# Kernel tuning notes

Measured on AMD Instinct MI355X. Metric: run time of the kernel, lower is better.

Reference implementation:

```python
import jax, jax.numpy as jnp
import numpy as np

B, T, V, D, C, d, TSZ, L, P = 8, 12, 512, 1, 128, 8, 3, 3, 12
BETA = TSZ - 1


def _gauss(emb, mu, isg):
    # Gaussian_component: sum over d of -0.5*(emb-mu)^2 * inv_sigma^2
    return jnp.sum(-0.5 * (emb - mu) ** 2 * isg ** 2, axis=-1)


def _gfs(h, fw, fb, gw, gb):
    # GFS: Conv2d(T->C, kernel (1,C)) over x[B,T,V,C] -> [B,C,V], then 1x1 GLU
    s = jnp.einsum('btvc,otc->bov', h, fw) + fb[None, :, None]
    g = jnp.einsum('bov,po->bpv', s, gw) + gb[None, :, None]
    lhs, rhs = jnp.split(g, 2, axis=1)
    return lhs * jax.nn.sigmoid(rhs)  # B,C,V


def _forward(x, sape, tape, srpe, trpe, zeros_x, zeros_tape, range_mask,
             input_w, input_b, fs0_fc_w, fs0_fc_b, fs0_glu_w, fs0_glu_b,
             mus, inv_sigmas, xproj_w, xproj_b, seproj_w, teproj_w, ln_g, ln_b,
             fs_fc_w, fs_fc_b, fs_glu_w, fs_glu_b, glu_w, glu_b, out_w, out_b):
    h = x @ input_w + input_b  # B,T,V,C (InputLayer)
    tape_pad = jnp.concatenate([zeros_tape, tape], axis=1)  # B,T+beta,1,d
    mask = range_mask.reshape(V, TSZ, V)  # [j, k, i]
    skips = [_gfs(h, fs0_fc_w, fs0_fc_b, fs0_glu_w, fs0_glu_b)]
    for l in range(L):
        h_pad = jnp.concatenate([zeros_x, h], axis=1)  # B,T+beta,V,C
        # all T shifted windows at once (vectorizes the per-timestep loop)
        xwin = jnp.stack([h_pad[:, k:k + T] for k in range(TSZ)], axis=2)     # B,T,k,V,C
        twin = jnp.stack([tape_pad[:, k:k + T] for k in range(TSZ)], axis=2)  # B,T,k,1,d
        mu, isg = mus[l], inv_sigmas[l]
        gi = _gauss(sape, mu[0], isg[0])              # (V,)   source node i
        gj = _gauss(sape, mu[1], isg[1])              # (V,)   target node j
        gti = _gauss(tape, mu[2], isg[2])[:, :, 0]    # (B,T)  tape_i
        gtj = _gauss(twin, mu[3], isg[3])[..., 0]     # (B,T,k) tape_j windows
        ge = _gauss(srpe, mu[4], isg[4])              # (V,V)  [i,j]
        gtr = _gauss(trpe, mu[5], isg[5])[:, 0]       # (k,)
        # log S[b,t,j,k,i]; original gaussian[b,k,i,j] -> reshape -> transpose gives S[b,j,(k,i)]
        logS = (gi[None, None, None, None, :] + gj[None, None, :, None, None]
                + gti[:, :, None, None, None] + gtj[:, :, None, :, None]
                + ge.T[None, None, :, None, :] + gtr[None, None, None, :, None])
        S = jnp.exp(logS) * mask[None, None]          # B,T,V(j),k,V(i)
        # STPGConv: bmm(S, x) over the (k,i) axis
        agg = jnp.einsum('btjki,btkic->btjc', S, xwin)  # B,T,V,C
        z = agg @ xproj_w[l] + xproj_b[l]               # B,T,V,2C
        z = z + sape @ seproj_w[l] + tape @ teproj_w[l]  # SE:(V,2C); TE:(B,T,1,2C) broadcasts over V
        mn = jnp.mean(z, axis=-1, keepdims=True)
        var = jnp.mean((z - mn) ** 2, axis=-1, keepdims=True)
        z = (z - mn) * jax.lax.rsqrt(var + 1e-5) * ln_g[l] + ln_b[l]
        lhs, rhs = jnp.split(z, 2, axis=-1)
        h = lhs * jax.nn.sigmoid(rhs)                   # B,T,V,C
        skips.append(_gfs(h, fs_fc_w[l], fs_fc_b[l], fs_glu_w[l], fs_glu_b[l]))
    hc = jnp.concatenate(skips, axis=1)                 # B,(L+1)*C,V
    g = jnp.einsum('bov,po->bpv', hc, glu_w) + glu_b[None, :, None]
    lhs, rhs = jnp.split(g, 2, axis=1)
    gated = lhs * jax.nn.sigmoid(rhs)                   # B,4C,V
    out = jnp.einsum('bov,po->bpv', gated, out_w) + out_b[None, :, None]  # B,P*D,V
    return out[:, :, :, None]                           # D==1 -> (B,P,V,1)


def setup_inputs() -> dict:
    key = jax.random.key(0)

    def nrm(i, shape, s=1.0):
        return s * jax.random.normal(jax.random.fold_in(key, i), shape, dtype=jnp.float32)

    inp = {
        'x': nrm(0, (B, T, V, D)),
        'sape': nrm(1, (V, d), 0.5),
        'tape': nrm(2, (B, T, 1, d), 0.5),
        'srpe': nrm(3, (V, V, d), 0.5),
        'trpe': nrm(4, (TSZ, 1, d), 0.5),
        'zeros_x': jnp.zeros((B, BETA, V, C), jnp.float32),
        'zeros_tape': jnp.zeros((B, BETA, 1, d), jnp.float32),
        'range_mask': (jax.random.uniform(jax.random.fold_in(key, 5), (V, TSZ * V)) < 0.7).astype(jnp.float32),
        'input_w': nrm(6, (D, C), 0.5),
        'input_b': jnp.zeros((C,), jnp.float32),
        'fs0_fc_w': nrm(7, (C, T, C), 1.0 / np.sqrt(T * C)),
        'fs0_fc_b': jnp.zeros((C,), jnp.float32),
        'fs0_glu_w': nrm(8, (2 * C, C), 1.0 / np.sqrt(C)),
        'fs0_glu_b': jnp.zeros((2 * C,), jnp.float32),
        'mus': nrm(9, (L, 6, d)),
        'inv_sigmas': nrm(10, (L, 6, d), 0.3),
        'xproj_w': nrm(11, (L, C, 2 * C), 1.0 / np.sqrt(C)),
        'xproj_b': jnp.zeros((L, 2 * C), jnp.float32),
        'seproj_w': nrm(12, (L, d, 2 * C), 1.0 / np.sqrt(d)),
        'teproj_w': nrm(13, (L, d, 2 * C), 1.0 / np.sqrt(d)),
        'ln_g': jnp.ones((L, 2 * C), jnp.float32),
        'ln_b': jnp.zeros((L, 2 * C), jnp.float32),
        'fs_fc_w': nrm(14, (L, C, T, C), 1.0 / np.sqrt(T * C)),
        'fs_fc_b': jnp.zeros((L, C), jnp.float32),
        'fs_glu_w': nrm(15, (L, 2 * C, C), 1.0 / np.sqrt(C)),
        'fs_glu_b': jnp.zeros((L, 2 * C), jnp.float32),
        'glu_w': nrm(16, (8 * C, 4 * C), 1.0 / np.sqrt(4 * C)),
        'glu_b': jnp.zeros((8 * C,), jnp.float32),
        'out_w': nrm(17, (P * D, 4 * C), 1.0 / np.sqrt(4 * C)),
        'out_b': jnp.zeros((P * D,), jnp.float32),
    }
    return inp


def reference(x, sape, tape, srpe, trpe, zeros_x, zeros_tape, range_mask,
              input_w, input_b, fs0_fc_w, fs0_fc_b, fs0_glu_w, fs0_glu_b,
              mus, inv_sigmas, xproj_w, xproj_b, seproj_w, teproj_w, ln_g, ln_b,
              fs_fc_w, fs_fc_b, fs_glu_w, fs_glu_b, glu_w, glu_b, out_w, out_b):
    return _forward(x, sape, tape, srpe, trpe, zeros_x, zeros_tape, range_mask,
                    input_w, input_b, fs0_fc_w, fs0_fc_b, fs0_glu_w, fs0_glu_b,
                    mus, inv_sigmas, xproj_w, xproj_b, seproj_w, teproj_w, ln_g, ln_b,
                    fs_fc_w, fs_fc_b, fs_glu_w, fs_glu_b, glu_w, glu_b, out_w, out_b)
```

## Files before the change

kernel.cpp:

```cpp
#include <hip/hip_runtime.h>
#include <cstddef>


#define BB 8
#define TT 12
#define VV 512
#define CC 128

typedef unsigned short ushort_t;
typedef float f32x4 __attribute__((ext_vector_type(4)));
typedef short bf16x8 __attribute__((ext_vector_type(8)));

__device__ __forceinline__ float sigmoidf_(float x){ return 1.0f/(1.0f+expf(-x)); }

__device__ __forceinline__ void split_bf16(float x, ushort_t& hi, ushort_t& lo){
  unsigned u = __float_as_uint(x);
  hi = (ushort_t)(u >> 16);
  float r = x - __uint_as_float(u & 0xFFFF0000u);
  lo = (ushort_t)(__float_as_uint(r) >> 16);
}

__device__ __forceinline__ float gauss8(const float* __restrict__ e,
                                        const float* __restrict__ mu,
                                        const float* __restrict__ sg){
  float a = 0.f;
  #pragma unroll
  for (int dd=0; dd<8; ++dd){
    float df = e[dd]-mu[dd];
    float s  = sg[dd];
    a = fmaf(-0.5f*df*df, s*s, a);
  }
  return a;
}

__global__ __launch_bounds__(256) void k_prep(
    const float* __restrict__ fs0_fc_w, const float* __restrict__ fs_fc_w,
    const float* __restrict__ fs0_glu_w, const float* __restrict__ fs_glu_w,
    const float* __restrict__ glu_w, const float* __restrict__ out_w,
    const float* __restrict__ xw, const float* __restrict__ sw,
    const float* __restrict__ tw, const float* __restrict__ xb2,
    float* __restrict__ fwT, float* __restrict__ gwT,
    float* __restrict__ gluT, float* __restrict__ outT,
    ushort_t* __restrict__ xcat_hi, ushort_t* __restrict__ xcat_lo){
  int job = blockIdx.y;
  int gid = blockIdx.x*256 + threadIdx.x;
  if (job < 4){
    if (gid >= 196608) return;
    const float* src = (job==0) ? fs0_fc_w : fs_fc_w + (size_t)(job-1)*196608;
    float* dst = fwT + (size_t)job*196608;
    int r = gid / 1536, c = gid % 1536;
    dst[(size_t)c*128 + r] = src[gid];
  } else if (job < 8){
    if (gid >= 32768) return;
    int sl = job-4;
    const float* src = (sl==0) ? fs0_glu_w : fs_glu_w + (size_t)(sl-1)*32768;
    float* dst = gwT + (size_t)sl*32768;
    int r = gid / 128, c = gid % 128;
    dst[(size_t)c*256 + r] = src[gid];
  } else if (job == 8){
    if (gid >= 524288) return;
    int r = gid / 512, c = gid % 512;
    gluT[(size_t)c*1024 + r] = glu_w[gid];
  } else if (job == 9){
    if (gid >= 6144) return;
    int r = gid / 512, c = gid % 512;
    outT[(size_t)c*12 + r] = out_w[gid];
  } else {
    if (gid >= 122880) return;
    int ll  = gid / 40960;
    int rem = gid - ll*40960;
    int col = rem / 160;
    int k   = rem - col*160;
    float val;
    if (k < 128)       val = xw[(size_t)ll*32768 + (size_t)k*256 + col];
    else if (k < 136)  val = sw[(size_t)ll*2048 + (size_t)(k-128)*256 + col];
    else if (k < 144)  val = tw[(size_t)ll*2048 + (size_t)(k-136)*256 + col];
    else if (k == 144) val = xb2[ll*256 + col];
    else               val = 0.f;
    ushort_t hi, lo; split_bf16(val, hi, lo);
    xcat_hi[gid] = hi;
    xcat_lo[gid] = lo;
  }
}

__global__ __launch_bounds__(256) void k_input(const float* __restrict__ x,
    const float* __restrict__ iw, const float* __restrict__ ib,
    float* __restrict__ hA, ushort_t* __restrict__ hhiT, ushort_t* __restrict__ hloT){
  int bt = blockIdx.x;
  int v0 = blockIdx.y*64;
  int c = threadIdx.x >> 1, half = threadIdx.x & 1;
  int vb = v0 + half*32;
  float wc = iw[c], bc = ib[c];
  const float* xp = x + (size_t)bt*VV + vb;
  float hv[32];
  #pragma unroll
  for (int u=0;u<32;++u) hv[u] = fmaf(xp[u], wc, bc);
  #pragma unroll
  for (int u=0;u<32;++u) hA[((size_t)bt*VV + vb + u)*CC + c] = hv[u];
  unsigned wh[16], wl[16];
  #pragma unroll
  for (int m=0;m<16;++m){
    ushort_t h0,l0,h1,l1;
    split_bf16(hv[2*m],   h0, l0);
    split_bf16(hv[2*m+1], h1, l1);
    wh[m] = (unsigned)h0 | ((unsigned)h1<<16);
    wl[m] = (unsigned)l0 | ((unsigned)l1<<16);
  }
  ushort_t* hp = hhiT + ((size_t)bt*CC + c)*VV + vb;
  ushort_t* lp = hloT + ((size_t)bt*CC + c)*VV + vb;
  #pragma unroll
  for (int q=0;q<4;++q){
    *(uint4*)(hp + q*8) = make_uint4(wh[q*4],wh[q*4+1],wh[q*4+2],wh[q*4+3]);
    *(uint4*)(lp + q*8) = make_uint4(wl[q*4],wl[q*4+1],wl[q*4+2],wl[q*4+3]);
  }
}

__global__ __launch_bounds__(256) void k_gfs1(const float* __restrict__ h,
    const float* __restrict__ fwT, float* __restrict__ s_part){
  int vt = blockIdx.x, b = blockIdx.y, ts = blockIdx.z;
  int tid = threadIdx.x;
  int v0 = vt*32;
  __shared__ float hT[32][34];
  int vtt = tid & 3, ot = tid >> 2;
  float acc[2][8];
  #pragma unroll
  for (int a=0;a<2;++a)
    #pragma unroll
    for (int u=0;u<8;++u) acc[a][u] = 0.f;

  for (int tt=0; tt<3; ++tt){
    int t = ts*3 + tt;
    const float* hbase = h + ((size_t)(b*TT+t)*VV)*CC;
    for (int cch=0; cch<4; ++cch){
      int c0 = cch*32;
      __syncthreads();
      { int vv = tid>>3, c4 = tid&7;
        float4 val = *(const float4*)(hbase + (size_t)(v0+vv)*CC + c0 + c4*4);
        hT[c4*4+0][vv]=val.x; hT[c4*4+1][vv]=val.y;
        hT[c4*4+2][vv]=val.z; hT[c4*4+3][vv]=val.w; }
      __syncthreads();
      const float* fwb = fwT + ((size_t)t*128 + c0)*128 + ot*2;
      for (int c=0;c<32;++c){
        float2 wv = *(const float2*)(fwb + (size_t)c*128);
        float hv[8];
        *(float4*)hv     = *(const float4*)&hT[c][vtt*8];
        *(float4*)(hv+4) = *(const float4*)&hT[c][vtt*8+4];
        #pragma unroll
        for (int u=0;u<8;++u){
          acc[0][u] = fmaf(wv.x, hv[u], acc[0][u]);
          acc[1][u] = fmaf(wv.y, hv[u], acc[1][u]);
        }
      }
    }
  }
  float* sp = s_part + (((size_t)ts*BB+b)*128 + ot*2)*VV + v0 + vtt*8;
  #pragma unroll
  for (int a=0;a<2;++a){
    *(float4*)(sp + (size_t)a*VV)     = *(float4*)&acc[a][0];
    *(float4*)(sp + (size_t)a*VV + 4) = *(float4*)&acc[a][4];
  }
}

__global__ __launch_bounds__(256) void k_gfs2(const float* __restrict__ s_part,
    const float* __restrict__ fb, const float* __restrict__ gwT,
    const float* __restrict__ gb, float* __restrict__ hc, int slot){
  int vt = blockIdx.x, b = blockIdx.y;
  int v0 = vt*32; int tid = threadIdx.x;
  __shared__ float sL[128][36];
  for (int u=0;u<16;++u){
    int lid = u*256 + tid; int o = lid>>5, vv = lid&31;
    float sum = fb[o];
    #pragma unroll
    for (int sp=0;sp<4;++sp)
      sum += s_part[(((size_t)sp*BB+b)*128 + o)*VV + v0 + vv];
    sL[o][vv] = sum;
  }
  __syncthreads();
  int oo = tid & 127, vg = tid >> 7;
  float accL[16], accR[16];
  #pragma unroll
  for (int u=0;u<16;++u){ accL[u]=0.f; accR[u]=0.f; }
  for (int op=0; op<128; ++op){
    float glv = gwT[(size_t)op*256 + oo];
    float grv = gwT[(size_t)op*256 + 128 + oo];
    float sv[16];
    #pragma unroll
    for (int q=0;q<4;++q) *(float4*)(sv+q*4) = *(const float4*)&sL[op][vg*16 + q*4];
    #pragma unroll
    for (int u=0;u<16;++u){ accL[u]=fmaf(glv,sv[u],accL[u]); accR[u]=fmaf(grv,sv[u],accR[u]); }
  }
  float bl = gb[oo], br = gb[128+oo];
  float outv[16];
  #pragma unroll
  for (int u=0;u<16;++u) outv[u] = (accL[u]+bl)*sigmoidf_(accR[u]+br);
  float* dst = hc + ((size_t)b*512 + slot*128 + oo)*VV + v0 + vg*16;
  #pragma unroll
  for (int q=0;q<4;++q) *(float4*)(dst+q*4) = *(float4*)(outv+q*4);
}

__global__ void k_smalls(const float* __restrict__ sape, const float* __restrict__ tape,
    const float* __restrict__ trpe, const float* __restrict__ mus,
    const float* __restrict__ isgs, int l,
    float* __restrict__ gi, float* __restrict__ gj,
    float* __restrict__ E, float* __restrict__ F, float* __restrict__ gtr){
  int tid = threadIdx.x;
  const float* mu = mus  + (size_t)l*48;
  const float* sg = isgs + (size_t)l*48;
  if (tid < 512){
    const float* e = sape + (size_t)tid*8;
    gi[tid] = gauss8(e, mu+0,  sg+0);
    gj[tid] = gauss8(e, mu+8,  sg+8);
  }
  if (tid < 96)
    E[tid] = expf(gauss8(tape + (size_t)tid*8, mu+16, sg+16));
  if (tid < 288){
    int k = tid % 3, bt = tid / 3;
    int t = bt % TT, b = bt / TT;
    int s = t + k - 2;
    F[tid] = (s >= 0) ? expf(gauss8(tape + (size_t)(b*TT+s)*8, mu+24, sg+24)) : 0.f;
  }
  if (tid < 3)
    gtr[tid] = gauss8(trpe + (size_t)tid*8, mu+40, sg+40);
}

__global__ __launch_bounds__(256) void k_W(const float* __restrict__ srpe,
    const float* __restrict__ mask, const float* __restrict__ mus,
    const float* __restrict__ isgs, int l,
    const float* __restrict__ gi, const float* __restrict__ gj,
    const float* __restrict__ gtr,
    ushort_t* __restrict__ Whi, ushort_t* __restrict__ Wlo){
  int it = blockIdx.x, jt = blockIdx.y;
  int tid = threadIdx.x;
  int ii = tid & 15, jj = tid >> 4;
  int i = it*16 + ii, j = jt*16 + jj;
  const float* mu = mus  + (size_t)l*48 + 32;
  const float* sg = isgs + (size_t)l*48 + 32;
  float ge = gauss8(srpe + ((size_t)i*VV + j)*8, mu, sg);
  float base = gi[i] + gj[j] + ge;
  float gk[3] = {gtr[0], gtr[1], gtr[2]};
  __shared__ unsigned tile[16][17];
  int arr = tid>>7, rem = tid&127, jr = rem>>3, p = rem&7;
  for (int k=0;k<3;++k){
    float m = mask[(size_t)j*1536 + k*512 + i];
    float val = m * expf(base + gk[k]);
    ushort_t hi, lo; split_bf16(val, hi, lo);
    __syncthreads();
    tile[jj][ii] = (unsigned)hi | ((unsigned)lo<<16);
    __syncthreads();
    unsigned w0 = tile[jr][2*p], w1 = tile[jr][2*p+1];
    unsigned outw = (arr==0) ? ((w0&0xFFFFu) | (w1<<16))
                             : ((w0>>16) | (w1&0xFFFF0000u));
    ushort_t* dst = (arr ? Wlo : Whi) + ((size_t)k*VV + jt*16 + jr)*VV + it*16 + 2*p;
    *(unsigned*)dst = outw;
  }
}

__global__ __launch_bounds__(256) void k_stpg(
    const ushort_t* __restrict__ hhiT, const ushort_t* __restrict__ hloT,
    const ushort_t* __restrict__ Whi,  const ushort_t* __restrict__ Wlo,
    const float* __restrict__ E, const float* __restrict__ F,
    float* __restrict__ agg){
  int bt = blockIdx.x; int b = bt/TT, t = bt - b*TT;
  int j0 = blockIdx.y * 128;
  int tid = threadIdx.x;
  int lane = tid & 63, wid = tid >> 6;
  int jw = (wid>>1)*64, cw = (wid&1)*64;

  __shared__ ushort_t Ahi_s[128*40];
  __shared__ ushort_t Alo_s[128*40];
  __shared__ ushort_t Bhi_s[128*40];
  __shared__ ushort_t Blo_s[128*40];

  f32x4 acc[4][4];
  #pragma unroll
  for (int a=0;a<4;++a)
    #pragma unroll
    for (int u=0;u<4;++u) acc[a][u] = (f32x4){0.f,0.f,0.f,0.f};

  int kmin = (t>=2) ? 0 : (2-t);
  float Fk[3] = {F[bt*3+0], F[bt*3+1], F[bt*3+2]};
  float Eb = E[bt];

  int ro = (lane&15)*40 + (lane>>4)*8;

  for (int k=kmin; k<3; ++k){
    int s = t + k - 2;
    const ushort_t* gAhi = Whi  + ((size_t)k*VV + j0)*VV;
    const ushort_t* gAlo = Wlo  + ((size_t)k*VV + j0)*VV;
    const ushort_t* gBhi = hhiT + (size_t)(b*TT+s)*CC*VV;
    const ushort_t* gBlo = hloT + (size_t)(b*TT+s)*CC*VV;
    for (int i0=0; i0<512; i0+=32){
      __syncthreads();
      #pragma unroll
      for (int p=0;p<2;++p){
        int sl = p*256 + tid;
        int r = sl>>2, q = sl&3;
        size_t go = (size_t)r*VV + i0 + q*8;
        int lo_ = r*40 + q*8;
        *(uint4*)&Ahi_s[lo_] = *(const uint4*)(gAhi + go);
        *(uint4*)&Alo_s[lo_] = *(const uint4*)(gAlo + go);
        *(uint4*)&Bhi_s[lo_] = *(const uint4*)(gBhi + go);
        *(uint4*)&Blo_s[lo_] = *(const uint4*)(gBlo + go);
      }
      __syncthreads();
      bf16x8 ah[4], al[4], bh[4], bl[4];
      #pragma unroll
      for (int f=0; f<4; ++f){
        ah[f] = *(const bf16x8*)&Ahi_s[(jw + f*16)*40 + ro];
        al[f] = *(const bf16x8*)&Alo_s[(jw + f*16)*40 + ro];
        bh[f] = *(const bf16x8*)&Bhi_s[(cw + f*16)*40 + ro];
        bl[f] = *(const bf16x8*)&Blo_s[(cw + f*16)*40 + ro];
      }
      #pragma unroll
      for (int jf=0;jf<4;++jf)
        #pragma unroll
        for (int cf=0;cf<4;++cf){
          acc[jf][cf] = __builtin_amdgcn_mfma_f32_16x16x32_bf16(ah[jf], bh[cf], acc[jf][cf],0,0,0);
          acc[jf][cf] = __builtin_amdgcn_mfma_f32_16x16x32_bf16(ah[jf], bl[cf], acc[jf][cf],0,0,0);
          acc[jf][cf] = __builtin_amdgcn_mfma_f32_16x16x32_bf16(al[jf], bh[cf], acc[jf][cf],0,0,0);
        }
    }
    if (k < 2){
      float r = Fk[k]/Fk[k+1];
      #pragma unroll
      for (int jf=0;jf<4;++jf)
        #pragma unroll
        for (int cf=0;cf<4;++cf) acc[jf][cf] *= r;
    }
  }
  float fin = Fk[2]*Eb;
  #pragma unroll
  for (int jf=0;jf<4;++jf){
    #pragma unroll
    for (int cf=0;cf<4;++cf){
      int row = j0 + jw + jf*16 + (lane>>4)*4;
      int col = cw + cf*16 + (lane&15);
      float* dst = agg + ((size_t)bt*VV + row)*CC + col;
      #pragma unroll
      for (int e=0;e<4;++e) dst[(size_t)e*CC] = acc[jf][cf][e]*fin;
    }
  }
}

__global__ __launch_bounds__(256,2) void k_xln2(
    float* __restrict__ hA,
    const ushort_t* __restrict__ xcat_hi, const ushort_t* __restrict__ xcat_lo,
    const float* __restrict__ sape, const float* __restrict__ tape,
    const float* __restrict__ lng, const float* __restrict__ lnb, int l,
    ushort_t* __restrict__ hhiT, ushort_t* __restrict__ hloT){
  int vt = blockIdx.x, bt = blockIdx.y;
  int v0 = vt*128;
  int tid = threadIdx.x;
  int lane = tid & 63, w = tid >> 6;
  int l15 = lane & 15, l4 = lane >> 4;
  int ko = l4*8;

  __shared__ float sef[128][8];
  __shared__ float tef[8];
  __shared__ float lnwS[256], lnbS[256];
  { int r2 = tid>>1, hh = tid&1;
    *(float4*)&sef[r2][hh*4] = *(const float4*)(sape + (size_t)(v0+r2)*8 + hh*4); }
  if (tid < 8) tef[tid] = tape[(size_t)bt*8 + tid];
  lnwS[tid] = lng[l*256 + tid];
  lnbS[tid] = lnb[l*256 + tid];
  __syncthreads();

  f32x4 acc[2][16];
  #pragma unroll
  for (int m=0;m<2;++m)
    #pragma unroll
    for (int n=0;n<16;++n) acc[m][n] = (f32x4){0.f,0.f,0.f,0.f};

  const ushort_t* bhb = xcat_hi + (size_t)l*40960;
  const ushort_t* blb = xcat_lo + (size_t)l*40960;

  #pragma unroll
  for (int ks=0; ks<5; ++ks){
    bf16x8 a_h[2], a_l[2];
    #pragma unroll
    for (int m=0;m<2;++m){
      int lrow = w*32 + m*16 + l15;
      float av[8];
      if (ks < 4){
        const float* ap = hA + ((size_t)bt*VV + v0 + lrow)*CC + ks*32 + ko;
        *(float4*)av     = *(const float4*)ap;
        *(float4*)(av+4) = *(const float4*)(ap+4);
      } else {
        #pragma unroll
        for (int u=0;u<8;++u) av[u] = 0.f;
        if (l4==0){
          #pragma unroll
          for (int u=0;u<8;++u) av[u] = sef[lrow][u];
        } else if (l4==1){
          #pragma unroll
          for (int u=0;u<8;++u) av[u] = tef[u];
        } else if (l4==2){
          av[0] = 1.f;
        }
      }
      #pragma unroll
      for (int u=0;u<8;++u){
        ushort_t hi, lo; split_bf16(av[u], hi, lo);
        a_h[m][u] = (short)hi; a_l[m][u] = (short)lo;
      }
    }
    #pragma unroll
    for (int n=0;n<16;++n){
      size_t boff = (size_t)(n*16 + l15)*160 + ks*32 + ko;
      bf16x8 b_h = *(const bf16x8*)(bhb + boff);
      bf16x8 b_l = *(const bf16x8*)(blb + boff);
      #pragma unroll
      for (int m=0;m<2;++m){
        acc[m][n] = __builtin_amdgcn_mfma_f32_16x16x32_bf16(a_h[m], b_h, acc[m][n],0,0,0);
        acc[m][n] = __builtin_amdgcn_mfma_f32_16x16x32_bf16(a_h[m], b_l, acc[m][n],0,0,0);
        acc[m][n] = __builtin_amdgcn_mfma_f32_16x16x32_bf16(a_l[m], b_h, acc[m][n],0,0,0);
      }
    }
  }

  float mn[2][4], rs[2][4];
  #pragma unroll
  for (int m=0;m<2;++m){
    #pragma unroll
    for (int e=0;e<4;++e){
      float s1=0.f, s2=0.f;
      #pragma unroll
      for (int n=0;n<16;++n){ float v = acc[m][n][e]; s1 += v; s2 = fmaf(v,v,s2); }
      #pragma unroll
      for (int off=8; off>=1; off>>=1){
        s1 += __shfl_xor(s1, off, 64);
        s2 += __shfl_xor(s2, off, 64);
      }
      float mu = s1*(1.f/256.f);
      mn[m][e] = mu;
      rs[m][e] = 1.f/sqrtf(s2*(1.f/256.f) - mu*mu + 1e-5f);
    }
  }

  float* hbase = hA + ((size_t)bt*VV)*CC;
  #pragma unroll
  for (int m=0;m<2;++m){
    #pragma unroll
    for (int n=0;n<8;++n){
      int cL = n*16 + l15, cR = cL + 128;
      float gL = lnwS[cL], bL = lnbS[cL];
      float gR = lnwS[cR], bR = lnbS[cR];
      ushort_t hi4[4], lo4[4];
      #pragma unroll
      for (int e=0;e<4;++e){
        float nl = (acc[m][n][e]   - mn[m][e])*rs[m][e]*gL + bL;
        float nr = (acc[m][n+8][e] - mn[m][e])*rs[m][e]*gR + bR;
        float hv = nl * sigmoidf_(nr);
        int v = v0 + w*32 + m*16 + l4*4 + e;
        hbase[(size_t)v*CC + cL] = hv;
        split_bf16(hv, hi4[e], lo4[e]);
      }
      int vbase = v0 + w*32 + m*16 + l4*4;
      ushort_t* hp = hhiT + ((size_t)bt*CC + cL)*VV + vbase;
      ushort_t* lp = hloT + ((size_t)bt*CC + cL)*VV + vbase;
      *(uint2*)hp = make_uint2((unsigned)hi4[0] | ((unsigned)hi4[1]<<16),
                               (unsigned)hi4[2] | ((unsigned)hi4[3]<<16));
      *(uint2*)lp = make_uint2((unsigned)lo4[0] | ((unsigned)lo4[1]<<16),
                               (unsigned)lo4[2] | ((unsigned)lo4[3]<<16));
    }
  }
}

__global__ __launch_bounds__(256) void k_final(const float* __restrict__ hc,
    const float* __restrict__ gluT, const float* __restrict__ glub,
    const float* __restrict__ outT, const float* __restrict__ outb,
    float* __restrict__ out){
  int b = blockIdx.y; int v0 = blockIdx.x * 8;
  int tid = threadIdx.x;
  __shared__ float hcl[512][8];
  __shared__ float gl[512][9];
  for (int u=0; u<16; ++u){
    int lid = u*256 + tid; int o = lid>>3, vv = lid&7;
    hcl[o][vv] = hc[((size_t)b*512 + o)*VV + v0 + vv];
  }
  __syncthreads();
  float aL0[8], aR0[8], aL1[8], aR1[8];
  #pragma unroll
  for (int u=0;u<8;++u){ aL0[u]=0.f; aR0[u]=0.f; aL1[u]=0.f; aR1[u]=0.f; }
  for (int o=0; o<512; ++o){
    const float* grow = gluT + (size_t)o*1024;
    float g0 = grow[tid], g1 = grow[tid+256], g2 = grow[tid+512], g3 = grow[tid+768];
    float hv[8];
    *(float4*)hv     = *(const float4*)&hcl[o][0];
    *(float4*)(hv+4) = *(const float4*)&hcl[o][4];
    #pragma unroll
    for (int u=0;u<8;++u){
      aL0[u]=fmaf(g0,hv[u],aL0[u]); aL1[u]=fmaf(g1,hv[u],aL1[u]);
      aR0[u]=fmaf(g2,hv[u],aR0[u]); aR1[u]=fmaf(g3,hv[u],aR1[u]);
    }
  }
  float bL0 = glub[tid], bL1 = glub[tid+256], bR0 = glub[tid+512], bR1 = glub[tid+768];
  #pragma unroll
  for (int u=0;u<8;++u){
    gl[tid][u]     = (aL0[u]+bL0)*sigmoidf_(aR0[u]+bR0);
    gl[tid+256][u] = (aL1[u]+bL1)*sigmoidf_(aR1[u]+bR1);
  }
  __syncthreads();
  if (tid < 96){
    int r = tid>>3, vv = tid&7;
    float acc = outb[r];
    for (int q=0; q<512; ++q) acc = fmaf(outT[(size_t)q*12 + r], gl[q][vv], acc);
    out[(size_t)b*6144 + r*512 + v0 + vv] = acc;
  }
}

extern "C" void kernel_launch(void* const* d_in, const int* in_sizes, int n_in,
                              void* d_out, int out_size, void* d_ws, size_t ws_size,
                              hipStream_t stream){
  const float* x        = (const float*)d_in[0];
  const float* sape     = (const float*)d_in[1];
  const float* tape     = (const float*)d_in[2];
  const float* srpe     = (const float*)d_in[3];
  const float* trpe     = (const float*)d_in[4];
  const float* mask     = (const float*)d_in[7];
  const float* input_w  = (const float*)d_in[8];
  const float* input_b  = (const float*)d_in[9];
  const float* fs0_fc_w = (const float*)d_in[10];
  const float* fs0_fc_b = (const float*)d_in[11];
  const float* fs0_glu_w= (const float*)d_in[12];
  const float* fs0_glu_b= (const float*)d_in[13];
  const float* mus      = (const float*)d_in[14];
  const float* isg      = (const float*)d_in[15];
  const float* xproj_w  = (const float*)d_in[16];
  const float* xproj_b  = (const float*)d_in[17];
  const float* seproj_w = (const float*)d_in[18];
  const float* teproj_w = (const float*)d_in[19];
  const float* ln_g     = (const float*)d_in[20];
  const float* ln_b     = (const float*)d_in[21];
  const float* fs_fc_w  = (const float*)d_in[22];
  const float* fs_fc_b  = (const float*)d_in[23];
  const float* fs_glu_w = (const float*)d_in[24];
  const float* fs_glu_b = (const float*)d_in[25];
  const float* glu_w    = (const float*)d_in[26];
  const float* glu_b    = (const float*)d_in[27];
  const float* out_w    = (const float*)d_in[28];
  const float* out_b    = (const float*)d_in[29];

  float* ws    = (float*)d_ws;
  float* hA    = ws;
  float* hc    = hA    + 6291456;
  float* s_part= hc    + 2097152;
  float* fwT   = s_part+ 2097152;
  float* gwT   = fwT   + 786432;
  float* gluT  = gwT   + 131072;
  float* outT  = gluT  + 524288;
  float* gi    = outT  + 6144;
  float* gj    = gi    + 512;
  float* Ebuf  = gj    + 512;
  float* Fbuf  = Ebuf  + 96;
  float* gtr   = Fbuf  + 288;
  ushort_t* hhiT = (ushort_t*)(gtr + 16);
  ushort_t* hloT = hhiT + 6291456;
  ushort_t* Whi  = hloT + 6291456;
  ushort_t* Wlo  = Whi  + 786432;
  ushort_t* xcat_hi = Wlo + 786432;
  ushort_t* xcat_lo = xcat_hi + 122880;

  k_prep<<<dim3(2048,11),256,0,stream>>>(fs0_fc_w, fs_fc_w, fs0_glu_w, fs_glu_w,
                                         glu_w, out_w, xproj_w, seproj_w, teproj_w,
                                         xproj_b, fwT, gwT, gluT, outT,
                                         xcat_hi, xcat_lo);
  k_input<<<dim3(96,8),256,0,stream>>>(x, input_w, input_b, hA, hhiT, hloT);
  k_gfs1<<<dim3(16,8,4),256,0,stream>>>(hA, fwT, s_part);
  k_gfs2<<<dim3(16,8),256,0,stream>>>(s_part, fs0_fc_b, gwT, fs0_glu_b, hc, 0);

  for (int l=0; l<3; ++l){
    k_smalls<<<1,512,0,stream>>>(sape, tape, trpe, mus, isg, l, gi, gj, Ebuf, Fbuf, gtr);
    k_W<<<dim3(32,32),256,0,stream>>>(srpe, mask, mus, isg, l, gi, gj, gtr, Whi, Wlo);
    k_stpg<<<dim3(96,4),256,0,stream>>>(hhiT, hloT, Whi, Wlo, Ebuf, Fbuf, hA);
    k_xln2<<<dim3(4,96),256,0,stream>>>(hA, xcat_hi, xcat_lo, sape, tape,
                                        ln_g, ln_b, l, hhiT, hloT);
    k_gfs1<<<dim3(16,8,4),256,0,stream>>>(hA, fwT + (size_t)(l+1)*196608, s_part);
    k_gfs2<<<dim3(16,8),256,0,stream>>>(s_part, fs_fc_b + l*128, gwT + (size_t)(l+1)*32768,
                                        fs_glu_b + l*256, hc, l+1);
  }
  k_final<<<dim3(64,8),256,0,stream>>>(hc, gluT, glu_b, outT, out_b, (float*)d_out);
}
```

Measured before the change: 877.6 us.

## Store W and h operands in MFMA fragment layout and drop LDS staging

The producers (k_input, k_xln2, k_W) now write the hi/lo bf16 split operands directly in a per-16x32 MFMA fragment-major layout, so k_stpg loads each lane's bf16x8 fragment straight from global memory. This removes the shared-memory tiles and the two barriers per K-step in the main aggregation GEMM, and k_W no longer needs an LDS transpose. The trade-off is that operand reuse across waves now goes through L2/L1 instead of LDS, and there is no explicit prefetch, so latency hiding depends on the cache.

```diff
diff --git a/kernel.cpp b/kernel.cpp
--- a/kernel.cpp
+++ b/kernel.cpp
@@ -85,7 +85,7 @@
 
 __global__ __launch_bounds__(256) void k_input(const float* __restrict__ x,
     const float* __restrict__ iw, const float* __restrict__ ib,
-    float* __restrict__ hA, ushort_t* __restrict__ hhiT, ushort_t* __restrict__ hloT){
+    float* __restrict__ hA, ushort_t* __restrict__ hfh, ushort_t* __restrict__ hfl){
   int bt = blockIdx.x;
   int v0 = blockIdx.y*64;
   int c = threadIdx.x >> 1, half = threadIdx.x & 1;
@@ -106,12 +106,14 @@
     wh[m] = (unsigned)h0 | ((unsigned)h1<<16);
     wl[m] = (unsigned)l0 | ((unsigned)l1<<16);
   }
-  ushort_t* hp = hhiT + ((size_t)bt*CC + c)*VV + vb;
-  ushort_t* lp = hloT + ((size_t)bt*CC + c)*VV + vb;
+  int ct = c>>4, c15 = c&15;
+  int ic = vb>>5;
+  size_t basea = (((size_t)bt*8 + ct)*16 + ic)*512;
   #pragma unroll
   for (int q=0;q<4;++q){
-    *(uint4*)(hp + q*8) = make_uint4(wh[q*4],wh[q*4+1],wh[q*4+2],wh[q*4+3]);
-    *(uint4*)(lp + q*8) = make_uint4(wl[q*4],wl[q*4+1],wl[q*4+2],wl[q*4+3]);
+    size_t off = basea + (size_t)(c15 + 16*q)*8;
+    *(uint4*)(hfh + off) = make_uint4(wh[q*4],wh[q*4+1],wh[q*4+2],wh[q*4+3]);
+    *(uint4*)(hfl + off) = make_uint4(wl[q*4],wl[q*4+1],wl[q*4+2],wl[q*4+3]);
   }
 }
 
@@ -228,48 +230,55 @@
     const float* __restrict__ isgs, int l,
     const float* __restrict__ gi, const float* __restrict__ gj,
     const float* __restrict__ gtr,
-    ushort_t* __restrict__ Whi, ushort_t* __restrict__ Wlo){
-  int it = blockIdx.x, jt = blockIdx.y;
+    ushort_t* __restrict__ Wfh, ushort_t* __restrict__ Wfl){
+  int ig = blockIdx.x;
+  int jt = blockIdx.y;
   int tid = threadIdx.x;
-  int ii = tid & 15, jj = tid >> 4;
-  int i = it*16 + ii, j = jt*16 + jj;
+  int jj = tid & 15, it8 = tid >> 4;
+  int j = jt*16 + jj;
+  int ib = ig*128 + it8*8;
   const float* mu = mus  + (size_t)l*48 + 32;
   const float* sg = isgs + (size_t)l*48 + 32;
-  float ge = gauss8(srpe + ((size_t)i*VV + j)*8, mu, sg);
-  float base = gi[i] + gj[j] + ge;
+  float gjv = gj[j];
+  float base[8];
+  #pragma unroll
+  for (int u=0;u<8;++u){
+    int i = ib + u;
+    base[u] = gi[i] + gjv + gauss8(srpe + ((size_t)i*VV + j)*8, mu, sg);
+  }
   float gk[3] = {gtr[0], gtr[1], gtr[2]};
-  __shared__ unsigned tile[16][17];
-  int arr = tid>>7, rem = tid&127, jr = rem>>3, p = rem&7;
+  int lane = jj + 16*((ib>>3)&3);
+  int ic = ib>>5;
   for (int k=0;k<3;++k){
-    float m = mask[(size_t)j*1536 + k*512 + i];
-    float val = m * expf(base + gk[k]);
-    ushort_t hi, lo; split_bf16(val, hi, lo);
-    __syncthreads();
-    tile[jj][ii] = (unsigned)hi | ((unsigned)lo<<16);
-    __syncthreads();
-    unsigned w0 = tile[jr][2*p], w1 = tile[jr][2*p+1];
-    unsigned outw = (arr==0) ? ((w0&0xFFFFu) | (w1<<16))
-                             : ((w0>>16) | (w1&0xFFFF0000u));
-    ushort_t* dst = (arr ? Wlo : Whi) + ((size_t)k*VV + jt*16 + jr)*VV + it*16 + 2*p;
-    *(unsigned*)dst = outw;
+    unsigned ph[4], pl[4];
+    #pragma unroll
+    for (int m=0;m<4;++m){
+      ushort_t h0,l0,h1,l1;
+      float m0 = mask[(size_t)j*1536 + k*512 + ib + 2*m];
+      float m1 = mask[(size_t)j*1536 + k*512 + ib + 2*m+1];
+      split_bf16(m0*expf(base[2*m]  +gk[k]), h0, l0);
+      split_bf16(m1*expf(base[2*m+1]+gk[k]), h1, l1);
+      ph[m] = (unsigned)h0 | ((unsigned)h1<<16);
+      pl[m] = (unsigned)l0 | ((unsigned)l1<<16);
+    }
+    size_t off = (((size_t)k*32 + jt)*16 + ic)*512 + (size_t)lane*8;
+    *(uint4*)(Wfh + off) = make_uint4(ph[0],ph[1],ph[2],ph[3]);
+    *(uint4*)(Wfl + off) = make_uint4(pl[0],pl[1],pl[2],pl[3]);
   }
 }
 
 __global__ __launch_bounds__(256) void k_stpg(
-    const ushort_t* __restrict__ hhiT, const ushort_t* __restrict__ hloT,
-    const ushort_t* __restrict__ Whi,  const ushort_t* __restrict__ Wlo,
+    const ushort_t* __restrict__ hfh, const ushort_t* __restrict__ hfl,
+    const ushort_t* __restrict__ Wfh,  const ushort_t* __restrict__ Wfl,
     const float* __restrict__ E, const float* __restrict__ F,
     float* __restrict__ agg){
   int bt = blockIdx.x; int b = bt/TT, t = bt - b*TT;
-  int j0 = blockIdx.y * 128;
   int tid = threadIdx.x;
   int lane = tid & 63, wid = tid >> 6;
-  int jw = (wid>>1)*64, cw = (wid&1)*64;
-
-  __shared__ ushort_t Ahi_s[128*40];
-  __shared__ ushort_t Alo_s[128*40];
-  __shared__ ushort_t Bhi_s[128*40];
-  __shared__ ushort_t Blo_s[128*40];
+  int wr = wid >> 1, wc = wid & 1;
+  int jtb = blockIdx.y*8 + wr*4;
+  int ctb = wc*4;
+  size_t lo8 = (size_t)lane*8;
 
   f32x4 acc[4][4];
   #pragma unroll
@@ -281,35 +290,22 @@
   float Fk[3] = {F[bt*3+0], F[bt*3+1], F[bt*3+2]};
   float Eb = E[bt];
 
-  int ro = (lane&15)*40 + (lane>>4)*8;
-
   for (int k=kmin; k<3; ++k){
     int s = t + k - 2;
-    const ushort_t* gAhi = Whi  + ((size_t)k*VV + j0)*VV;
-    const ushort_t* gAlo = Wlo  + ((size_t)k*VV + j0)*VV;
-    const ushort_t* gBhi = hhiT + (size_t)(b*TT+s)*CC*VV;
-    const ushort_t* gBlo = hloT + (size_t)(b*TT+s)*CC*VV;
-    for (int i0=0; i0<512; i0+=32){
-      __syncthreads();
-      #pragma unroll
-      for (int p=0;p<2;++p){
-        int sl = p*256 + tid;
-        int r = sl>>2, q = sl&3;
-        size_t go = (size_t)r*VV + i0 + q*8;
-        int lo_ = r*40 + q*8;
-        *(uint4*)&Ahi_s[lo_] = *(const uint4*)(gAhi + go);
-        *(uint4*)&Alo_s[lo_] = *(const uint4*)(gAlo + go);
-        *(uint4*)&Bhi_s[lo_] = *(const uint4*)(gBhi + go);
-        *(uint4*)&Blo_s[lo_] = *(const uint4*)(gBlo + go);
-      }
-      __syncthreads();
+    const ushort_t* Ah = Wfh + ((size_t)k*32*16)*512;
+    const ushort_t* Al = Wfl + ((size_t)k*32*16)*512;
+    const ushort_t* Bh = hfh + (((size_t)(b*TT+s))*8*16)*512;
+    const ushort_t* Bl = hfl + (((size_t)(b*TT+s))*8*16)*512;
+    for (int ic=0; ic<16; ++ic){
       bf16x8 ah[4], al[4], bh[4], bl[4];
       #pragma unroll
       for (int f=0; f<4; ++f){
-        ah[f] = *(const bf16x8*)&Ahi_s[(jw + f*16)*40 + ro];
-        al[f] = *(const bf16x8*)&Alo_s[(jw + f*16)*40 + ro];
-        bh[f] = *(const bf16x8*)&Bhi_s[(cw + f*16)*40 + ro];
-        bl[f] = *(const bf16x8*)&Blo_s[(cw + f*16)*40 + ro];
+        size_t ao = (((size_t)(jtb+f)*16 + ic)*512) + lo8;
+        size_t bo = (((size_t)(ctb+f)*16 + ic)*512) + lo8;
+        ah[f] = *(const bf16x8*)(Ah + ao);
+        al[f] = *(const bf16x8*)(Al + ao);
+        bh[f] = *(const bf16x8*)(Bh + bo);
+        bl[f] = *(const bf16x8*)(Bl + bo);
       }
       #pragma unroll
       for (int jf=0;jf<4;++jf)
@@ -333,8 +329,8 @@
   for (int jf=0;jf<4;++jf){
     #pragma unroll
     for (int cf=0;cf<4;++cf){
-      int row = j0 + jw + jf*16 + (lane>>4)*4;
-      int col = cw + cf*16 + (lane&15);
+      int row = blockIdx.y*128 + wr*64 + jf*16 + (lane>>4)*4;
+      int col = wc*64 + cf*16 + (lane&15);
       float* dst = agg + ((size_t)bt*VV + row)*CC + col;
       #pragma unroll
       for (int e=0;e<4;++e) dst[(size_t)e*CC] = acc[jf][cf][e]*fin;
@@ -347,7 +343,7 @@
     const ushort_t* __restrict__ xcat_hi, const ushort_t* __restrict__ xcat_lo,
     const float* __restrict__ sape, const float* __restrict__ tape,
     const float* __restrict__ lng, const float* __restrict__ lnb, int l,
-    ushort_t* __restrict__ hhiT, ushort_t* __restrict__ hloT){
+    ushort_t* __restrict__ hfh, ushort_t* __restrict__ hfl){
   int vt = blockIdx.x, bt = blockIdx.y;
   int v0 = vt*128;
   int tid = threadIdx.x;
@@ -438,8 +434,14 @@
   }
 
   float* hbase = hA + ((size_t)bt*VV)*CC;
+  int ic = vt*4 + w;
+  int qq = (2*0 + (l4>>1)) & 3;
+  (void)qq;
   #pragma unroll
   for (int m=0;m<2;++m){
+    int q = (2*m + (l4>>1)) & 3;
+    int lane2 = l15 + 16*q;
+    int uoff = (l4 & 1)*4;
     #pragma unroll
     for (int n=0;n<8;++n){
       int cL = n*16 + l15, cR = cL + 128;
@@ -455,13 +457,11 @@
         hbase[(size_t)v*CC + cL] = hv;
         split_bf16(hv, hi4[e], lo4[e]);
       }
-      int vbase = v0 + w*32 + m*16 + l4*4;
-      ushort_t* hp = hhiT + ((size_t)bt*CC + cL)*VV + vbase;
-      ushort_t* lp = hloT + ((size_t)bt*CC + cL)*VV + vbase;
-      *(uint2*)hp = make_uint2((unsigned)hi4[0] | ((unsigned)hi4[1]<<16),
-                               (unsigned)hi4[2] | ((unsigned)hi4[3]<<16));
-      *(uint2*)lp = make_uint2((unsigned)lo4[0] | ((unsigned)lo4[1]<<16),
-                               (unsigned)lo4[2] | ((unsigned)lo4[3]<<16));
+      size_t off = (((size_t)bt*8 + n)*16 + ic)*512 + (size_t)lane2*8 + uoff;
+      *(uint2*)(hfh + off) = make_uint2((unsigned)hi4[0] | ((unsigned)hi4[1]<<16),
+                                        (unsigned)hi4[2] | ((unsigned)hi4[3]<<16));
+      *(uint2*)(hfl + off) = make_uint2((unsigned)lo4[0] | ((unsigned)lo4[1]<<16),
+                                        (unsigned)lo4[2] | ((unsigned)lo4[3]<<16));
     }
   }
 }
@@ -554,27 +554,27 @@
   float* Ebuf  = gj    + 512;
   float* Fbuf  = Ebuf  + 96;
   float* gtr   = Fbuf  + 288;
-  ushort_t* hhiT = (ushort_t*)(gtr + 16);
-  ushort_t* hloT = hhiT + 6291456;
-  ushort_t* Whi  = hloT + 6291456;
-  ushort_t* Wlo  = Whi  + 786432;
-  ushort_t* xcat_hi = Wlo + 786432;
+  ushort_t* hfh  = (ushort_t*)(gtr + 16);
+  ushort_t* hfl  = hfh + 6291456;
+  ushort_t* Wfh  = hfl + 6291456;
+  ushort_t* Wfl  = Wfh + 786432;
+  ushort_t* xcat_hi = Wfl + 786432;
   ushort_t* xcat_lo = xcat_hi + 122880;
 
   k_prep<<<dim3(2048,11),256,0,stream>>>(fs0_fc_w, fs_fc_w, fs0_glu_w, fs_glu_w,
                                          glu_w, out_w, xproj_w, seproj_w, teproj_w,
                                          xproj_b, fwT, gwT, gluT, outT,
                                          xcat_hi, xcat_lo);
-  k_input<<<dim3(96,8),256,0,stream>>>(x, input_w, input_b, hA, hhiT, hloT);
+  k_input<<<dim3(96,8),256,0,stream>>>(x, input_w, input_b, hA, hfh, hfl);
   k_gfs1<<<dim3(16,8,4),256,0,stream>>>(hA, fwT, s_part);
   k_gfs2<<<dim3(16,8),256,0,stream>>>(s_part, fs0_fc_b, gwT, fs0_glu_b, hc, 0);
 
   for (int l=0; l<3; ++l){
     k_smalls<<<1,512,0,stream>>>(sape, tape, trpe, mus, isg, l, gi, gj, Ebuf, Fbuf, gtr);
-    k_W<<<dim3(32,32),256,0,stream>>>(srpe, mask, mus, isg, l, gi, gj, gtr, Whi, Wlo);
-    k_stpg<<<dim3(96,4),256,0,stream>>>(hhiT, hloT, Whi, Wlo, Ebuf, Fbuf, hA);
+    k_W<<<dim3(4,32),256,0,stream>>>(srpe, mask, mus, isg, l, gi, gj, gtr, Wfh, Wfl);
+    k_stpg<<<dim3(96,4),256,0,stream>>>(hfh, hfl, Wfh, Wfl, Ebuf, Fbuf, hA);
     k_xln2<<<dim3(4,96),256,0,stream>>>(hA, xcat_hi, xcat_lo, sape, tape,
-                                        ln_g, ln_b, l, hhiT, hloT);
+                                        ln_g, ln_b, l, hfh, hfl);
     k_gfs1<<<dim3(16,8,4),256,0,stream>>>(hA, fwT + (size_t)(l+1)*196608, s_part);
     k_gfs2<<<dim3(16,8),256,0,stream>>>(s_part, fs_fc_b + l*128, gwT + (size_t)(l+1)*32768,
                                         fs_glu_b + l*256, hc, l+1);
```

Result: no change. 894.7 us (+2.0%).
